# Optimization experiments

Hardware: AMD Instinct MI355X
Metric: run time of the kernel (lower is better)

Reference implementation:

```python
import jax, jax.numpy as jnp
import numpy as np

N = 50000      # nodes
E = 250000     # edges (pairs) per key
DIN = 256
DOUT = 256
OH = 16        # one_hot_length
T = 2          # params['t']


def setup_inputs() -> dict:
    key = jax.random.key(0)
    ks = jax.random.split(key, 16)
    s_in = 1.0 / np.float32(np.sqrt(DIN))
    s_tr = 1.0 / np.float32(np.sqrt(DIN + OH))
    return {
        "h": jax.random.normal(ks[0], (N, DIN), jnp.float32),
        "pairs_k0": jax.random.randint(ks[1], (T, E), 0, N),
        "pairs_k1": jax.random.randint(ks[2], (T, E), 0, N),
        "degrees_k0": jax.random.uniform(ks[3], (T, E, OH), jnp.float32),
        "degrees_k1": jax.random.uniform(ks[4], (T, E, OH), jnp.float32),
        "scatter_k0": jax.random.randint(ks[5], (E,), 0, N),
        "scatter_k1": jax.random.randint(ks[6], (E,), 0, N),
        "W_lin": jax.random.normal(ks[7], (DIN, DOUT), jnp.float32) * s_in,
        "b_lin": jax.random.normal(ks[8], (DOUT,), jnp.float32) * 0.01,
        "W_k0": jax.random.normal(ks[9], (DIN + OH, DOUT), jnp.float32) * s_tr,
        "b_k0": jax.random.normal(ks[10], (DOUT,), jnp.float32) * 0.01,
        "W_k1": jax.random.normal(ks[11], (DIN + OH, DOUT), jnp.float32) * s_tr,
        "b_k1": jax.random.normal(ks[12], (DOUT,), jnp.float32) * 0.01,
        "eps_k0": jnp.zeros((1,), jnp.float32),
        "eps_k1": jnp.zeros((1,), jnp.float32),
    }


def _key_term(h, pairs, degrees, W, b, scatter, eps):
    # combination == 'multi': product over t of sigmoid(Linear([h[pairs_i], deg_i]))
    h_temp = jnp.ones((pairs.shape[1], W.shape[1]), h.dtype)
    for i in range(T):
        h_t = jnp.concatenate([h[pairs[i]], degrees[i]], axis=1)  # [E, DIN+OH]
        h_temp = h_temp * jax.nn.sigmoid(h_t @ W + b)             # [E, DOUT]
    h_sum = jax.ops.segment_sum(h_temp, scatter, num_segments=N)  # [N, DOUT]
    return (1.0 + eps) * h_sum                                    # scalar eps (shape [1])


def reference(h, pairs_k0, pairs_k1, degrees_k0, degrees_k1,
              scatter_k0, scatter_k1, W_lin, b_lin,
              W_k0, b_k0, W_k1, b_k1, eps_k0, eps_k1):
    h3 = h @ W_lin + b_lin
    h3 = h3 + _key_term(h, pairs_k0, degrees_k0, W_k0, b_k0, scatter_k0, eps_k0)
    h3 = h3 + _key_term(h, pairs_k1, degrees_k1, W_k1, b_k1, scatter_k1, eps_k1)
    return h3
```

## Files before the change

### kernel.cpp

```cpp
#include <hip/hip_runtime.h>
#include <hip/hip_bf16.h>

#define N_NODES 50000
#define N_EDGES 250000
#define DIN_ 256
#define DOUT_ 256
#define OH_ 16
#define KF_ 288
#define NBLK_EDGE ((N_EDGES + 63) / 64)
#define NBLK_G ((N_NODES + 63) / 64)
#define SCAN_TOT (2 * N_NODES)
#define SCAN_NB ((SCAN_TOT + 255) / 256)

typedef short short8 __attribute__((ext_vector_type(8)));
typedef float f32x4 __attribute__((ext_vector_type(4)));

__device__ __forceinline__ unsigned short f2bf(float f) {
    unsigned u = __builtin_bit_cast(unsigned, f);
    return (unsigned short)((u + 0x7fffu + ((u >> 16) & 1u)) >> 16);
}

__device__ __forceinline__ float bf2f(unsigned short v) {
    return __builtin_bit_cast(float, (unsigned)v << 16);
}

__device__ __forceinline__ uint4 pack8(float f0, float f1, float f2, float f3,
                                       float f4, float f5, float f6, float f7) {
    uint4 u;
    u.x = (unsigned)f2bf(f0) | ((unsigned)f2bf(f1) << 16);
    u.y = (unsigned)f2bf(f2) | ((unsigned)f2bf(f3) << 16);
    u.z = (unsigned)f2bf(f4) | ((unsigned)f2bf(f5) << 16);
    u.w = (unsigned)f2bf(f6) | ((unsigned)f2bf(f7) << 16);
    return u;
}

__device__ __forceinline__ float fast_rcp(float x) {
#if __has_builtin(__builtin_amdgcn_rcpf)
    return __builtin_amdgcn_rcpf(x);
#else
    return 1.0f / x;
#endif
}

__device__ __forceinline__ void gl_lds16(const void* g, void* l) {
    __builtin_amdgcn_global_load_lds(
        (const __attribute__((address_space(1))) unsigned int*)g,
        (__attribute__((address_space(3))) unsigned int*)l, 16, 0, 0);
}

__global__ void hist_kernel(const int* __restrict__ sc0, const int* __restrict__ sc1,
                            int* __restrict__ hist) {
    int e = blockIdx.x * 256 + threadIdx.x;
    if (e < N_EDGES) {
        atomicAdd(&hist[sc0[e]], 1);
        atomicAdd(&hist[N_NODES + sc1[e]], 1);
    }
}

__global__ void scan_pass1(const int* __restrict__ hist, int* __restrict__ partials) {
    __shared__ int sdata[256];
    int gid = blockIdx.x * 256 + threadIdx.x;
    sdata[threadIdx.x] = (gid < SCAN_TOT) ? hist[gid] : 0;
    __syncthreads();
    for (int d = 128; d > 0; d >>= 1) {
        if (threadIdx.x < d) sdata[threadIdx.x] += sdata[threadIdx.x + d];
        __syncthreads();
    }
    if (threadIdx.x == 0) partials[blockIdx.x] = sdata[0];
}

__global__ __launch_bounds__(512) void scan_pass2(int* __restrict__ partials) {
    __shared__ int s[512];
    int t = threadIdx.x;
    s[t] = (t < SCAN_NB) ? partials[t] : 0;
    __syncthreads();
    for (int d = 1; d < 512; d <<= 1) {
        int add = (t >= d) ? s[t - d] : 0;
        __syncthreads();
        s[t] += add;
        __syncthreads();
    }
    if (t < SCAN_NB) partials[t] = (t == 0) ? 0 : s[t - 1];
}

__global__ void scan_pass3(const int* __restrict__ hist, const int* __restrict__ partials,
                           int* __restrict__ offs) {
    __shared__ int s[256];
    int gid = blockIdx.x * 256 + threadIdx.x;
    int t = threadIdx.x;
    int v = (gid < SCAN_TOT) ? hist[gid] : 0;
    s[t] = v;
    __syncthreads();
    for (int d = 1; d < 256; d <<= 1) {
        int add = (t >= d) ? s[t - d] : 0;
        __syncthreads();
        s[t] += add;
        __syncthreads();
    }
    if (gid < SCAN_TOT) offs[gid] = partials[blockIdx.x] + s[t] - v;
}

__global__ void rank_kernel(const int* __restrict__ sc0, const int* __restrict__ sc1,
                            int* __restrict__ offs, int* __restrict__ order,
                            int* __restrict__ keys) {
    int e = blockIdx.x * 256 + threadIdx.x;
    if (e < N_EDGES) {
        int k0 = sc0[e];
        int p = atomicAdd(&offs[k0], 1);
        order[p] = e; keys[p] = k0;
        int k1 = sc1[e];
        int q = atomicAdd(&offs[N_NODES + k1], 1);
        order[q] = e; keys[q] = k1;
    }
}

__global__ void prep_weights(const float* __restrict__ W_lin,
                             const float* __restrict__ W_k0,
                             const float* __restrict__ W_k1,
                             unsigned short* __restrict__ WT_lin,
                             unsigned short* __restrict__ WT_k0,
                             unsigned short* __restrict__ WT_k1) {
    int idx = blockIdx.x * 256 + threadIdx.x;
    if (idx < DOUT_ * DIN_) {
        int n = idx >> 8, k = idx & 255;
        WT_lin[idx] = f2bf(W_lin[k * DOUT_ + n]);
    }
    if (idx < DOUT_ * KF_) {
        int n = idx / KF_, k = idx - n * KF_;
        float v0 = 0.f, v1 = 0.f;
        if (k < DIN_ + OH_) {
            v0 = W_k0[k * DOUT_ + n];
            v1 = W_k1[k * DOUT_ + n];
        }
        WT_k0[idx] = f2bf(v0);
        WT_k1[idx] = f2bf(v1);
    }
}

__global__ void conv_h(const float* __restrict__ h, unsigned short* __restrict__ hbf) {
    int idx = blockIdx.x * 256 + threadIdx.x;
    const float4* s = (const float4*)(h + (size_t)idx * 8);
    float4 a = s[0], b = s[1];
    ((uint4*)hbf)[idx] = pack8(a.x, a.y, a.z, a.w, b.x, b.y, b.z, b.w);
}

__global__ __launch_bounds__(256) void main_gemm(const unsigned short* __restrict__ hbf,
                                                 const unsigned short* __restrict__ WT,
                                                 const float* __restrict__ bias,
                                                 float* __restrict__ out) {
    __shared__ unsigned short Alds[2][64][32];
    __shared__ unsigned short Blds[2][256][32];
    __shared__ float bias_lds[256];
    int tid = threadIdx.x;
    int w = tid >> 6, ln = tid & 63, l15 = ln & 15;
    int row0 = blockIdx.x * 64;
    bias_lds[tid] = bias[tid];

    int ar = row0 + w * 16 + (ln >> 2);
    if (ar >= N_NODES) ar = N_NODES - 1;
    int qs = (ln & 3) ^ ((ln >> 3) & 3);
    const unsigned short* asrc = hbf + (size_t)ar * DIN_ + qs * 8;
    int brow = w * 64;
    int swz = ((ln >> 4) ^ ((l15 >> 1) & 3)) * 8;

    f32x4 acc[16];
#pragma unroll
    for (int j = 0; j < 16; ++j) acc[j] = (f32x4)(0.f);

    gl_lds16(asrc, &Alds[0][w * 16][0]);
#pragma unroll
    for (int i = 0; i < 4; ++i) {
        int n = brow + i * 16 + (ln >> 2);
        gl_lds16(WT + (size_t)n * DIN_ + qs * 8, &Blds[0][brow + i * 16][0]);
    }
    __syncthreads();

    int buf = 0;
    for (int kk = 0; kk < 8; ++kk) {
        if (kk < 7) {
            gl_lds16(asrc + (kk + 1) * 32, &Alds[buf ^ 1][w * 16][0]);
#pragma unroll
            for (int i = 0; i < 4; ++i) {
                int n = brow + i * 16 + (ln >> 2);
                gl_lds16(WT + (size_t)n * DIN_ + (kk + 1) * 32 + qs * 8,
                         &Blds[buf ^ 1][brow + i * 16][0]);
            }
        }
        short8 af = *(const short8*)&Alds[buf][w * 16 + l15][swz];
#pragma unroll
        for (int j = 0; j < 16; ++j) {
            short8 bf = *(const short8*)&Blds[buf][j * 16 + l15][swz];
            acc[j] = __builtin_amdgcn_mfma_f32_16x16x32_bf16(af, bf, acc[j], 0, 0, 0);
        }
        __syncthreads();
        buf ^= 1;
    }

    int rbase = row0 + w * 16 + ((ln >> 4) << 2);
#pragma unroll
    for (int j = 0; j < 16; ++j) {
        int n = j * 16 + l15;
        float bv = bias_lds[n];
#pragma unroll
        for (int i = 0; i < 4; ++i) {
            int rr = rbase + i;
            if (rr < N_NODES) out[(size_t)rr * DOUT_ + n] = acc[j][i] + bv;
        }
    }
}

__global__ __launch_bounds__(256) void g_gemm(const unsigned short* __restrict__ hbf,
                                              const unsigned short* __restrict__ WT0,
                                              const unsigned short* __restrict__ WT1,
                                              const float* __restrict__ b0,
                                              const float* __restrict__ b1,
                                              unsigned short* __restrict__ G0,
                                              unsigned short* __restrict__ G1) {
    __shared__ unsigned short Alds[2][64][32];
    __shared__ unsigned short Blds[2][256][32];
    __shared__ float bias_lds[256];
    int kb = (blockIdx.x >= NBLK_G) ? 1 : 0;
    int bx = blockIdx.x - kb * NBLK_G;
    const unsigned short* WT = kb ? WT1 : WT0;
    const float* bias = kb ? b1 : b0;
    unsigned short* G = kb ? G1 : G0;

    int tid = threadIdx.x;
    int w = tid >> 6, ln = tid & 63, l15 = ln & 15;
    int row0 = bx * 64;
    bias_lds[tid] = bias[tid];

    int ar = row0 + w * 16 + (ln >> 2);
    if (ar >= N_NODES) ar = N_NODES - 1;
    int qs = (ln & 3) ^ ((ln >> 3) & 3);
    const unsigned short* asrc = hbf + (size_t)ar * DIN_ + qs * 8;
    int brow = w * 64;
    int swz = ((ln >> 4) ^ ((l15 >> 1) & 3)) * 8;

    f32x4 acc[16];
#pragma unroll
    for (int j = 0; j < 16; ++j) acc[j] = (f32x4)(0.f);

    gl_lds16(asrc, &Alds[0][w * 16][0]);
#pragma unroll
    for (int i = 0; i < 4; ++i) {
        int n = brow + i * 16 + (ln >> 2);
        gl_lds16(WT + (size_t)n * KF_ + qs * 8, &Blds[0][brow + i * 16][0]);
    }
    __syncthreads();

    int buf = 0;
    for (int kk = 0; kk < 8; ++kk) {
        if (kk < 7) {
            gl_lds16(asrc + (kk + 1) * 32, &Alds[buf ^ 1][w * 16][0]);
#pragma unroll
            for (int i = 0; i < 4; ++i) {
                int n = brow + i * 16 + (ln >> 2);
                gl_lds16(WT + (size_t)n * KF_ + (kk + 1) * 32 + qs * 8,
                         &Blds[buf ^ 1][brow + i * 16][0]);
            }
        }
        short8 af = *(const short8*)&Alds[buf][w * 16 + l15][swz];
#pragma unroll
        for (int j = 0; j < 16; ++j) {
            short8 bf = *(const short8*)&Blds[buf][j * 16 + l15][swz];
            acc[j] = __builtin_amdgcn_mfma_f32_16x16x32_bf16(af, bf, acc[j], 0, 0, 0);
        }
        __syncthreads();
        buf ^= 1;
    }

    int rbase = row0 + w * 16 + ((ln >> 4) << 2);
#pragma unroll
    for (int j = 0; j < 16; ++j) {
        int n = j * 16 + l15;
        float bv = bias_lds[n];
#pragma unroll
        for (int i = 0; i < 4; ++i) {
            int rr = rbase + i;
            if (rr < N_NODES) G[(size_t)rr * DOUT_ + n] = f2bf(acc[j][i] + bv);
        }
    }
}

__global__ __launch_bounds__(256) void edge_fused(const unsigned short* __restrict__ Gk0,
                                                  const unsigned short* __restrict__ Gk1,
                                                  const int* __restrict__ pairs0,
                                                  const int* __restrict__ pairs1,
                                                  const float* __restrict__ deg0,
                                                  const float* __restrict__ deg1,
                                                  const int* __restrict__ order_all,
                                                  const int* __restrict__ keys_all,
                                                  const unsigned short* __restrict__ WT0,
                                                  const unsigned short* __restrict__ WT1,
                                                  const float* __restrict__ eps0,
                                                  const float* __restrict__ eps1,
                                                  float* __restrict__ out) {
    __shared__ float red0[64][68];
    __shared__ float red1[64][68];
    __shared__ int tgt[64], pl0[64], pl1[64], el[64];
    int kb = (blockIdx.x >= NBLK_EDGE) ? 1 : 0;
    int bx = blockIdx.x - kb * NBLK_EDGE;
    const unsigned short* G = kb ? Gk1 : Gk0;
    const int* pairs = kb ? pairs1 : pairs0;
    const float* degrees = kb ? deg1 : deg0;
    const int* order_k = order_all + kb * N_EDGES;
    const int* keys_k  = keys_all + kb * N_EDGES;
    const unsigned short* WT = kb ? WT1 : WT0;
    float epv = 1.0f + (kb ? eps1[0] : eps0[0]);

    int tid = threadIdx.x;
    int w = tid >> 6, ln = tid & 63, l15 = ln & 15, ks = ln >> 4;
    int e0 = bx * 64;
    if (tid < 64) {
        int s = e0 + tid;
        int sc = (s < N_EDGES) ? s : N_EDGES - 1;
        int e = order_k[sc];
        el[tid]  = e;
        tgt[tid] = (s < N_EDGES) ? keys_k[s] : -1;
        pl0[tid] = pairs[e];
        pl1[tid] = pairs[N_EDGES + e];
    }
    __syncthreads();

    int eA = el[w * 16 + l15];
    short8 a0f = (short8)0, a1f = (short8)0;
    if (ks < 2) {
        const float4* s0 = (const float4*)(degrees + ((size_t)0 * N_EDGES + eA) * OH_ + ks * 8);
        const float4* s1 = (const float4*)(degrees + ((size_t)1 * N_EDGES + eA) * OH_ + ks * 8);
        float4 xa = s0[0], xb = s0[1];
        float4 ya = s1[0], yb = s1[1];
        a0f = __builtin_bit_cast(short8, pack8(xa.x, xa.y, xa.z, xa.w, xb.x, xb.y, xb.z, xb.w));
        a1f = __builtin_bit_cast(short8, pack8(ya.x, ya.y, ya.z, ya.w, yb.x, yb.y, yb.z, yb.w));
    }

    int c = ln;
    int Rb = w * 16;

#pragma unroll
    for (int half = 0; half < 2; ++half) {
        f32x4 acc0[8], acc1[8];
#pragma unroll
        for (int j = 0; j < 8; ++j) { acc0[j] = (f32x4)(0.f); acc1[j] = (f32x4)(0.f); }
#pragma unroll
        for (int j = 0; j < 8; ++j) {
            int n = half * 128 + j * 16 + l15;
            short8 bf = (short8)0;
            if (ks < 2) bf = *(const short8*)(WT + (size_t)n * KF_ + 256 + ks * 8);
            acc0[j] = __builtin_amdgcn_mfma_f32_16x16x32_bf16(a0f, bf, acc0[j], 0, 0, 0);
            acc1[j] = __builtin_amdgcn_mfma_f32_16x16x32_bf16(a1f, bf, acc1[j], 0, 0, 0);
        }
#pragma unroll
        for (int jc = 0; jc < 2; ++jc) {
#pragma unroll
            for (int jj = 0; jj < 4; ++jj) {
#pragma unroll
                for (int i = 0; i < 4; ++i) {
                    int row = w * 16 + ks * 4 + i;
                    red0[row][jj * 16 + l15] = acc0[jc * 4 + jj][i];
                    red1[row][jj * 16 + l15] = acc1[jc * 4 + jj][i];
                }
            }
            __syncthreads();
            int n = half * 128 + jc * 64 + c;
            int runkey = tgt[Rb];
            float runsum;
            {
                float g0 = bf2f(G[(size_t)pl0[Rb] * DOUT_ + n]);
                float g1 = bf2f(G[(size_t)pl1[Rb] * DOUT_ + n]);
                float ea = __expf(-(g0 + red0[Rb][c]));
                float eb = __expf(-(g1 + red1[Rb][c]));
                runsum = epv * fast_rcp((1.f + ea) * (1.f + eb));
            }
#pragma unroll
            for (int rr = 1; rr < 16; ++rr) {
                int r = Rb + rr;
                float g0 = bf2f(G[(size_t)pl0[r] * DOUT_ + n]);
                float g1 = bf2f(G[(size_t)pl1[r] * DOUT_ + n]);
                float ea = __expf(-(g0 + red0[r][c]));
                float eb = __expf(-(g1 + red1[r][c]));
                float val = epv * fast_rcp((1.f + ea) * (1.f + eb));
                int k = tgt[r];
                if (k != runkey) {
                    if (runkey >= 0) atomicAdd(&out[(size_t)runkey * DOUT_ + n], runsum);
                    runkey = k;
                    runsum = val;
                } else {
                    runsum += val;
                }
            }
            if (runkey >= 0) atomicAdd(&out[(size_t)runkey * DOUT_ + n], runsum);
            __syncthreads();
        }
    }
}

extern "C" void kernel_launch(void* const* d_in, const int* in_sizes, int n_in,
                              void* d_out, int out_size, void* d_ws, size_t ws_size,
                              hipStream_t stream) {
    const float* h        = (const float*)d_in[0];
    const int*   pairs_k0 = (const int*)d_in[1];
    const int*   pairs_k1 = (const int*)d_in[2];
    const float* deg_k0   = (const float*)d_in[3];
    const float* deg_k1   = (const float*)d_in[4];
    const int*   sc_k0    = (const int*)d_in[5];
    const int*   sc_k1    = (const int*)d_in[6];
    const float* W_lin    = (const float*)d_in[7];
    const float* b_lin    = (const float*)d_in[8];
    const float* W_k0     = (const float*)d_in[9];
    const float* b_k0     = (const float*)d_in[10];
    const float* W_k1     = (const float*)d_in[11];
    const float* b_k1     = (const float*)d_in[12];
    const float* eps_k0   = (const float*)d_in[13];
    const float* eps_k1   = (const float*)d_in[14];
    float* out = (float*)d_out;

    size_t ush_elems = (size_t)DOUT_ * DIN_ + 2 * (size_t)DOUT_ * KF_
                     + 3 * (size_t)N_NODES * DIN_;
    size_t int_elems = 2 * (size_t)N_NODES * 2 + 2 * (size_t)N_EDGES * 2 + 512;
    size_t need = ush_elems * sizeof(unsigned short) + int_elems * sizeof(int);
    if (ws_size < need) return;

    unsigned short* WT_lin = (unsigned short*)d_ws;
    unsigned short* WT_k0  = WT_lin + DOUT_ * DIN_;
    unsigned short* WT_k1  = WT_k0 + DOUT_ * KF_;
    unsigned short* h_bf   = WT_k1 + DOUT_ * KF_;
    unsigned short* G0     = h_bf + (size_t)N_NODES * DIN_;
    unsigned short* G1     = G0 + (size_t)N_NODES * DIN_;
    int* hist     = (int*)(G1 + (size_t)N_NODES * DIN_);
    int* offs     = hist + 2 * N_NODES;
    int* order    = offs + 2 * N_NODES;
    int* keys     = order + 2 * N_EDGES;
    int* partials = keys + 2 * N_EDGES;

    hipMemsetAsync(hist, 0, 2 * N_NODES * sizeof(int), stream);
    hist_kernel<<<(N_EDGES + 255) / 256, 256, 0, stream>>>(sc_k0, sc_k1, hist);
    scan_pass1<<<SCAN_NB, 256, 0, stream>>>(hist, partials);
    scan_pass2<<<1, 512, 0, stream>>>(partials);
    scan_pass3<<<SCAN_NB, 256, 0, stream>>>(hist, partials, offs);
    rank_kernel<<<(N_EDGES + 255) / 256, 256, 0, stream>>>(sc_k0, sc_k1, offs, order, keys);

    prep_weights<<<(DOUT_ * KF_ + 255) / 256, 256, 0, stream>>>(W_lin, W_k0, W_k1,
                                                                WT_lin, WT_k0, WT_k1);
    conv_h<<<(N_NODES * DIN_ / 8) / 256, 256, 0, stream>>>(h, h_bf);
    main_gemm<<<NBLK_G, 256, 0, stream>>>(h_bf, WT_lin, b_lin, out);
    g_gemm<<<2 * NBLK_G, 256, 0, stream>>>(h_bf, WT_k0, WT_k1, b_k0, b_k1, G0, G1);
    edge_fused<<<2 * NBLK_EDGE, 256, 0, stream>>>(G0, G1, pairs_k0, pairs_k1,
                                                  deg_k0, deg_k1, order, keys,
                                                  WT_k0, WT_k1, eps_k0, eps_k1, out);
}
```

Before: 427.1 us.

## Merge node GEMMs into one launch and restructure edge kernel reduction

Merges the linear GEMM and the two per-key G GEMMs into a single launch that picks weights and output by block index. In the edge kernel, each lane now handles two adjacent columns and loads paired bf16 gathers of G into registers up front; the second half's gathers are issued before the first reduction so their latency overlaps it. The degree-MFMA partials are stored to LDS as bf16 instead of fp32, which cuts LDS use and barrier count. Atomic flushes are reshuffled through a small LDS buffer so the adds stay coalesced by column. The costs are more register pressure and an extra bf16 rounding of the degree contribution.

```diff
diff --git a/kernel.cpp b/kernel.cpp
--- a/kernel.cpp
+++ b/kernel.cpp
@@ -20,8 +20,8 @@
     return (unsigned short)((u + 0x7fffu + ((u >> 16) & 1u)) >> 16);
 }
 
-__device__ __forceinline__ float bf2f(unsigned short v) {
-    return __builtin_bit_cast(float, (unsigned)v << 16);
+__device__ __forceinline__ float bf2f(unsigned v) {
+    return __builtin_bit_cast(float, v << 16);
 }
 
 __device__ __forceinline__ uint4 pack8(float f0, float f1, float f2, float f3,
@@ -144,16 +144,29 @@
     ((uint4*)hbf)[idx] = pack8(a.x, a.y, a.z, a.w, b.x, b.y, b.z, b.w);
 }
 
-__global__ __launch_bounds__(256) void main_gemm(const unsigned short* __restrict__ hbf,
-                                                 const unsigned short* __restrict__ WT,
-                                                 const float* __restrict__ bias,
-                                                 float* __restrict__ out) {
+__global__ __launch_bounds__(256) void lin_gemms(const unsigned short* __restrict__ hbf,
+                                                 const unsigned short* __restrict__ WT_lin,
+                                                 const unsigned short* __restrict__ WTk0,
+                                                 const unsigned short* __restrict__ WTk1,
+                                                 const float* __restrict__ b_lin,
+                                                 const float* __restrict__ bk0,
+                                                 const float* __restrict__ bk1,
+                                                 float* __restrict__ out,
+                                                 unsigned short* __restrict__ G0,
+                                                 unsigned short* __restrict__ G1) {
     __shared__ unsigned short Alds[2][64][32];
     __shared__ unsigned short Blds[2][256][32];
     __shared__ float bias_lds[256];
+    int kb = blockIdx.x / NBLK_G;
+    int bx = blockIdx.x - kb * NBLK_G;
+    const unsigned short* WT; const float* bias; int stride;
+    if (kb == 0)      { WT = WTk0;   bias = bk0;   stride = KF_; }
+    else if (kb == 1) { WT = WTk1;   bias = bk1;   stride = KF_; }
+    else              { WT = WT_lin; bias = b_lin; stride = DIN_; }
+
     int tid = threadIdx.x;
     int w = tid >> 6, ln = tid & 63, l15 = ln & 15;
-    int row0 = blockIdx.x * 64;
+    int row0 = bx * 64;
     bias_lds[tid] = bias[tid];
 
     int ar = row0 + w * 16 + (ln >> 2);
@@ -171,7 +184,7 @@
 #pragma unroll
     for (int i = 0; i < 4; ++i) {
         int n = brow + i * 16 + (ln >> 2);
-        gl_lds16(WT + (size_t)n * DIN_ + qs * 8, &Blds[0][brow + i * 16][0]);
+        gl_lds16(WT + (size_t)n * stride + qs * 8, &Blds[0][brow + i * 16][0]);
     }
     __syncthreads();
 
@@ -182,7 +195,7 @@
 #pragma unroll
             for (int i = 0; i < 4; ++i) {
                 int n = brow + i * 16 + (ln >> 2);
-                gl_lds16(WT + (size_t)n * DIN_ + (kk + 1) * 32 + qs * 8,
+                gl_lds16(WT + (size_t)n * stride + (kk + 1) * 32 + qs * 8,
                          &Blds[buf ^ 1][brow + i * 16][0]);
             }
         }
@@ -197,6 +210,7 @@
     }
 
     int rbase = row0 + w * 16 + ((ln >> 4) << 2);
+    unsigned short* G = (kb == 0) ? G0 : G1;
 #pragma unroll
     for (int j = 0; j < 16; ++j) {
         int n = j * 16 + l15;
@@ -204,81 +218,11 @@
 #pragma unroll
         for (int i = 0; i < 4; ++i) {
             int rr = rbase + i;
-            if (rr < N_NODES) out[(size_t)rr * DOUT_ + n] = acc[j][i] + bv;
-        }
-    }
-}
-
-__global__ __launch_bounds__(256) void g_gemm(const unsigned short* __restrict__ hbf,
-                                              const unsigned short* __restrict__ WT0,
-                                              const unsigned short* __restrict__ WT1,
-                                              const float* __restrict__ b0,
-                                              const float* __restrict__ b1,
-                                              unsigned short* __restrict__ G0,
-                                              unsigned short* __restrict__ G1) {
-    __shared__ unsigned short Alds[2][64][32];
-    __shared__ unsigned short Blds[2][256][32];
-    __shared__ float bias_lds[256];
-    int kb = (blockIdx.x >= NBLK_G) ? 1 : 0;
-    int bx = blockIdx.x - kb * NBLK_G;
-    const unsigned short* WT = kb ? WT1 : WT0;
-    const float* bias = kb ? b1 : b0;
-    unsigned short* G = kb ? G1 : G0;
-
-    int tid = threadIdx.x;
-    int w = tid >> 6, ln = tid & 63, l15 = ln & 15;
-    int row0 = bx * 64;
-    bias_lds[tid] = bias[tid];
-
-    int ar = row0 + w * 16 + (ln >> 2);
-    if (ar >= N_NODES) ar = N_NODES - 1;
-    int qs = (ln & 3) ^ ((ln >> 3) & 3);
-    const unsigned short* asrc = hbf + (size_t)ar * DIN_ + qs * 8;
-    int brow = w * 64;
-    int swz = ((ln >> 4) ^ ((l15 >> 1) & 3)) * 8;
-
-    f32x4 acc[16];
-#pragma unroll
-    for (int j = 0; j < 16; ++j) acc[j] = (f32x4)(0.f);
-
-    gl_lds16(asrc, &Alds[0][w * 16][0]);
-#pragma unroll
-    for (int i = 0; i < 4; ++i) {
-        int n = brow + i * 16 + (ln >> 2);
-        gl_lds16(WT + (size_t)n * KF_ + qs * 8, &Blds[0][brow + i * 16][0]);
-    }
-    __syncthreads();
-
-    int buf = 0;
-    for (int kk = 0; kk < 8; ++kk) {
-        if (kk < 7) {
-            gl_lds16(asrc + (kk + 1) * 32, &Alds[buf ^ 1][w * 16][0]);
-#pragma unroll
-            for (int i = 0; i < 4; ++i) {
-                int n = brow + i * 16 + (ln >> 2);
-                gl_lds16(WT + (size_t)n * KF_ + (kk + 1) * 32 + qs * 8,
-                         &Blds[buf ^ 1][brow + i * 16][0]);
+            if (rr < N_NODES) {
+                float v = acc[j][i] + bv;
+                if (kb == 2) out[(size_t)rr * DOUT_ + n] = v;
+                else         G[(size_t)rr * DOUT_ + n] = f2bf(v);
             }
-        }
-        short8 af = *(const short8*)&Alds[buf][w * 16 + l15][swz];
-#pragma unroll
-        for (int j = 0; j < 16; ++j) {
-            short8 bf = *(const short8*)&Blds[buf][j * 16 + l15][swz];
-            acc[j] = __builtin_amdgcn_mfma_f32_16x16x32_bf16(af, bf, acc[j], 0, 0, 0);
-        }
-        __syncthreads();
-        buf ^= 1;
-    }
-
-    int rbase = row0 + w * 16 + ((ln >> 4) << 2);
-#pragma unroll
-    for (int j = 0; j < 16; ++j) {
-        int n = j * 16 + l15;
-        float bv = bias_lds[n];
-#pragma unroll
-        for (int i = 0; i < 4; ++i) {
-            int rr = rbase + i;
-            if (rr < N_NODES) G[(size_t)rr * DOUT_ + n] = f2bf(acc[j][i] + bv);
         }
     }
 }
@@ -296,8 +240,8 @@
                                                   const float* __restrict__ eps0,
                                                   const float* __restrict__ eps1,
                                                   float* __restrict__ out) {
-    __shared__ float red0[64][68];
-    __shared__ float red1[64][68];
+    __shared__ unsigned short Dlds[2][64][132];
+    __shared__ float FL[4][64][2];
     __shared__ int tgt[64], pl0[64], pl1[64], el[64];
     int kb = (blockIdx.x >= NBLK_EDGE) ? 1 : 0;
     int bx = blockIdx.x - kb * NBLK_EDGE;
@@ -323,76 +267,104 @@
     }
     __syncthreads();
 
+    unsigned int gv00[16], gv10[16];
+#pragma unroll
+    for (int r = 0; r < 16; ++r) {
+        int row = w * 16 + r;
+        gv00[r] = *(const unsigned int*)(G + (size_t)pl0[row] * DOUT_ + 2 * ln);
+        gv10[r] = *(const unsigned int*)(G + (size_t)pl1[row] * DOUT_ + 2 * ln);
+    }
+
     int eA = el[w * 16 + l15];
     short8 a0f = (short8)0, a1f = (short8)0;
     if (ks < 2) {
-        const float4* s0 = (const float4*)(degrees + ((size_t)0 * N_EDGES + eA) * OH_ + ks * 8);
-        const float4* s1 = (const float4*)(degrees + ((size_t)1 * N_EDGES + eA) * OH_ + ks * 8);
+        const float4* s0 = (const float4*)(degrees + (size_t)eA * OH_ + ks * 8);
+        const float4* s1 = (const float4*)(degrees + ((size_t)N_EDGES + eA) * OH_ + ks * 8);
         float4 xa = s0[0], xb = s0[1];
         float4 ya = s1[0], yb = s1[1];
         a0f = __builtin_bit_cast(short8, pack8(xa.x, xa.y, xa.z, xa.w, xb.x, xb.y, xb.z, xb.w));
         a1f = __builtin_bit_cast(short8, pack8(ya.x, ya.y, ya.z, ya.w, yb.x, yb.y, yb.z, yb.w));
     }
 
-    int c = ln;
-    int Rb = w * 16;
-
-#pragma unroll
-    for (int half = 0; half < 2; ++half) {
-        f32x4 acc0[8], acc1[8];
-#pragma unroll
-        for (int j = 0; j < 8; ++j) { acc0[j] = (f32x4)(0.f); acc1[j] = (f32x4)(0.f); }
-#pragma unroll
-        for (int j = 0; j < 8; ++j) {
-            int n = half * 128 + j * 16 + l15;
-            short8 bf = (short8)0;
-            if (ks < 2) bf = *(const short8*)(WT + (size_t)n * KF_ + 256 + ks * 8);
-            acc0[j] = __builtin_amdgcn_mfma_f32_16x16x32_bf16(a0f, bf, acc0[j], 0, 0, 0);
-            acc1[j] = __builtin_amdgcn_mfma_f32_16x16x32_bf16(a1f, bf, acc1[j], 0, 0, 0);
-        }
-#pragma unroll
-        for (int jc = 0; jc < 2; ++jc) {
-#pragma unroll
-            for (int jj = 0; jj < 4; ++jj) {
-#pragma unroll
-                for (int i = 0; i < 4; ++i) {
-                    int row = w * 16 + ks * 4 + i;
-                    red0[row][jj * 16 + l15] = acc0[jc * 4 + jj][i];
-                    red1[row][jj * 16 + l15] = acc1[jc * 4 + jj][i];
-                }
-            }
-            __syncthreads();
-            int n = half * 128 + jc * 64 + c;
-            int runkey = tgt[Rb];
-            float runsum;
-            {
-                float g0 = bf2f(G[(size_t)pl0[Rb] * DOUT_ + n]);
-                float g1 = bf2f(G[(size_t)pl1[Rb] * DOUT_ + n]);
-                float ea = __expf(-(g0 + red0[Rb][c]));
-                float eb = __expf(-(g1 + red1[Rb][c]));
-                runsum = epv * fast_rcp((1.f + ea) * (1.f + eb));
-            }
-#pragma unroll
-            for (int rr = 1; rr < 16; ++rr) {
-                int r = Rb + rr;
-                float g0 = bf2f(G[(size_t)pl0[r] * DOUT_ + n]);
-                float g1 = bf2f(G[(size_t)pl1[r] * DOUT_ + n]);
-                float ea = __expf(-(g0 + red0[r][c]));
-                float eb = __expf(-(g1 + red1[r][c]));
-                float val = epv * fast_rcp((1.f + ea) * (1.f + eb));
-                int k = tgt[r];
-                if (k != runkey) {
-                    if (runkey >= 0) atomicAdd(&out[(size_t)runkey * DOUT_ + n], runsum);
-                    runkey = k;
-                    runsum = val;
-                } else {
-                    runsum += val;
-                }
-            }
-            if (runkey >= 0) atomicAdd(&out[(size_t)runkey * DOUT_ + n], runsum);
-            __syncthreads();
-        }
-    }
+#define MFMA_PHASE(p)                                                                  \
+    {                                                                                  \
+        f32x4 acc0[8], acc1[8];                                                        \
+        _Pragma("unroll")                                                              \
+        for (int j = 0; j < 8; ++j) { acc0[j] = (f32x4)(0.f); acc1[j] = (f32x4)(0.f); }\
+        _Pragma("unroll")                                                              \
+        for (int j = 0; j < 8; ++j) {                                                  \
+            int n = (p) * 128 + j * 16 + l15;                                          \
+            short8 bf = (short8)0;                                                     \
+            if (ks < 2) bf = *(const short8*)(WT + (size_t)n * KF_ + 256 + ks * 8);    \
+            acc0[j] = __builtin_amdgcn_mfma_f32_16x16x32_bf16(a0f, bf, acc0[j], 0,0,0);\
+            acc1[j] = __builtin_amdgcn_mfma_f32_16x16x32_bf16(a1f, bf, acc1[j], 0,0,0);\
+        }                                                                              \
+        _Pragma("unroll")                                                              \
+        for (int j = 0; j < 8; ++j) {                                                  \
+            _Pragma("unroll")                                                          \
+            for (int i = 0; i < 4; ++i) {                                              \
+                int row = w * 16 + ks * 4 + i;                                         \
+                Dlds[0][row][j * 16 + l15] = f2bf(acc0[j][i]);                         \
+                Dlds[1][row][j * 16 + l15] = f2bf(acc1[j][i]);                         \
+            }                                                                          \
+        }                                                                              \
+    }
+
+#define FLUSH(p, key, r0, r1)                                                          \
+    if ((key) >= 0) {                                                                  \
+        FL[w][ln][0] = (r0);                                                           \
+        FL[w][ln][1] = (r1);                                                           \
+        float va = FL[w][(ln >> 1)][ln & 1];                                           \
+        float vb = FL[w][32 + (ln >> 1)][ln & 1];                                      \
+        atomicAdd(&out[(size_t)(key) * DOUT_ + (p) * 128 + ln], va);                   \
+        atomicAdd(&out[(size_t)(key) * DOUT_ + (p) * 128 + 64 + ln], vb);              \
+    }
+
+#define REDUCE_PHASE(p, gva, gvb)                                                      \
+    {                                                                                  \
+        int runkey = tgt[w * 16];                                                      \
+        float rs0 = 0.f, rs1 = 0.f;                                                    \
+        _Pragma("unroll")                                                              \
+        for (int r = 0; r < 16; ++r) {                                                 \
+            int row = w * 16 + r;                                                      \
+            unsigned int d0u = *(const unsigned int*)&Dlds[0][row][2 * ln];            \
+            unsigned int d1u = *(const unsigned int*)&Dlds[1][row][2 * ln];            \
+            unsigned int g0u = gva[r], g1u = gvb[r];                                   \
+            float la0 = bf2f(g0u & 0xffffu) + bf2f(d0u & 0xffffu);                     \
+            float ha0 = bf2f(g0u >> 16) + bf2f(d0u >> 16);                             \
+            float la1 = bf2f(g1u & 0xffffu) + bf2f(d1u & 0xffffu);                     \
+            float ha1 = bf2f(g1u >> 16) + bf2f(d1u >> 16);                             \
+            float v0 = epv * fast_rcp((1.f + __expf(-la0)) * (1.f + __expf(-la1)));    \
+            float v1 = epv * fast_rcp((1.f + __expf(-ha0)) * (1.f + __expf(-ha1)));    \
+            int k = tgt[row];                                                          \
+            if (k != runkey) {                                                         \
+                FLUSH(p, runkey, rs0, rs1);                                            \
+                runkey = k; rs0 = v0; rs1 = v1;                                        \
+            } else { rs0 += v0; rs1 += v1; }                                           \
+        }                                                                              \
+        FLUSH(p, runkey, rs0, rs1);                                                    \
+    }
+
+    MFMA_PHASE(0);
+
+    unsigned int gv01[16], gv11[16];
+#pragma unroll
+    for (int r = 0; r < 16; ++r) {
+        int row = w * 16 + r;
+        gv01[r] = *(const unsigned int*)(G + (size_t)pl0[row] * DOUT_ + 128 + 2 * ln);
+        gv11[r] = *(const unsigned int*)(G + (size_t)pl1[row] * DOUT_ + 128 + 2 * ln);
+    }
+
+    __syncthreads();
+    REDUCE_PHASE(0, gv00, gv10);
+    __syncthreads();
+    MFMA_PHASE(1);
+    __syncthreads();
+    REDUCE_PHASE(1, gv01, gv11);
+
+#undef MFMA_PHASE
+#undef FLUSH
+#undef REDUCE_PHASE
 }
 
 extern "C" void kernel_launch(void* const* d_in, const int* in_sizes, int n_in,
@@ -443,8 +415,8 @@
     prep_weights<<<(DOUT_ * KF_ + 255) / 256, 256, 0, stream>>>(W_lin, W_k0, W_k1,
                                                                 WT_lin, WT_k0, WT_k1);
     conv_h<<<(N_NODES * DIN_ / 8) / 256, 256, 0, stream>>>(h, h_bf);
-    main_gemm<<<NBLK_G, 256, 0, stream>>>(h_bf, WT_lin, b_lin, out);
-    g_gemm<<<2 * NBLK_G, 256, 0, stream>>>(h_bf, WT_k0, WT_k1, b_k0, b_k1, G0, G1);
+    lin_gemms<<<3 * NBLK_G, 256, 0, stream>>>(h_bf, WT_lin, WT_k0, WT_k1,
+                                              b_lin, b_k0, b_k1, out, G0, G1);
     edge_fused<<<2 * NBLK_EDGE, 256, 0, stream>>>(G0, G1, pairs_k0, pairs_k1,
                                                   deg_k0, deg_k1, order, keys,
                                                   WT_k0, WT_k1, eps_k0, eps_k1, out);
```

Result: faster. 373.7 us (-12.5%).
